# Kernel optimization log

Hardware: AMD Instinct MI355X
Metric: run time of the kernel (lower is better)

The kernel has to match this reference:

```python
import jax, jax.numpy as jnp
import numpy as np

SCALE_POS = 2.0
SCALE_NEG = 40.0
THRESH_POS = 0.5
THRESH_NEG = 0.5
MARGIN = 0.1
EPS = 1e-5


def setup_inputs() -> dict:
    key = jax.random.key(0)
    kf, kl = jax.random.split(key)
    B, D, NUM_CLASSES = 4096, 1024, 64
    feats = jax.random.normal(kf, (B, D), dtype=jnp.float32)
    feats = feats / jnp.linalg.norm(feats, axis=1, keepdims=True)  # L2-normalized embeddings
    labels = jax.random.randint(kl, (B,), 0, NUM_CLASSES, dtype=jnp.int64)
    return {"feats": feats, "labels": labels}


def reference(feats, labels):
    B = feats.shape[0]
    sim = jnp.matmul(feats, feats.T)  # [B, B]
    same = labels[:, None] == labels[None, :]
    pos_mask = same & (sim < 1.0 - EPS)  # drop self / near-duplicate pairs
    neg_mask = ~same

    # hard mining: keep negatives above min positive - margin, positives below max negative + margin
    min_pos = jnp.min(jnp.where(pos_mask, sim, jnp.inf), axis=1)   # [B]
    max_neg = jnp.max(jnp.where(neg_mask, sim, -jnp.inf), axis=1)  # [B]
    neg_sel = neg_mask & (sim + MARGIN > min_pos[:, None])
    pos_sel = pos_mask & (sim - MARGIN < max_neg[:, None])

    pos_sum = jnp.sum(jnp.where(pos_sel, jnp.exp(-SCALE_POS * (sim - THRESH_POS)), 0.0), axis=1)
    neg_sum = jnp.sum(jnp.where(neg_sel, jnp.exp(SCALE_NEG * (sim - THRESH_NEG)), 0.0), axis=1)
    pos_loss = jnp.log1p(pos_sum) / SCALE_POS
    neg_loss = jnp.log1p(neg_sum) / SCALE_NEG

    valid = jnp.any(pos_sel, axis=1) & jnp.any(neg_sel, axis=1)  # rows skipped by original loop
    return jnp.sum(jnp.where(valid, pos_loss + neg_loss, 0.0)) / B
```

## Files before the change

### kernel.cpp

```cpp
#include <hip/hip_runtime.h>

typedef short short8 __attribute__((ext_vector_type(8)));
typedef _Float16 half8 __attribute__((ext_vector_type(8)));
typedef float floatx4 __attribute__((ext_vector_type(4)));
typedef __attribute__((address_space(1))) const void gvoid;
typedef __attribute__((address_space(3))) void svoid;

#define SCALE_POS 2.0f
#define SCALE_NEG 40.0f
#define THRESH 0.5f
#define MARGIN 0.1f
#define EPSV 1e-5f

__device__ __forceinline__ unsigned short f2bf(float f) {
    unsigned u = __float_as_uint(f);
    u += 0x7fffu + ((u >> 16) & 1u);
    return (unsigned short)(u >> 16);
}
__device__ __forceinline__ unsigned f2ord(float f) {
    unsigned u = __float_as_uint(f);
    return (u & 0x80000000u) ? ~u : (u | 0x80000000u);
}
__device__ __forceinline__ float ord2f(unsigned e) {
    unsigned v = (e & 0x80000000u) ? (e & 0x7fffffffu) : ~e;
    return __uint_as_float(v);
}

#define ORD_POS_INF 0xff800000u
#define ORD_NEG_INF 0x007fffffu

__global__ void k_init(const float* __restrict__ feats,
                       unsigned short* __restrict__ fb16,
                       unsigned* __restrict__ minp, unsigned* __restrict__ maxn,
                       float* __restrict__ psum, float* __restrict__ nsum,
                       unsigned* __restrict__ cnts,
                       int total4, int B) {
    int i = blockIdx.x * blockDim.x + threadIdx.x;
    if (i < total4) {
        float4 v = ((const float4*)feats)[i];
        ushort4 o;
        o.x = f2bf(v.x); o.y = f2bf(v.y); o.z = f2bf(v.z); o.w = f2bf(v.w);
        ((ushort4*)fb16)[i] = o;
    }
    if (i < B) {
        minp[i] = ORD_POS_INF;
        maxn[i] = ORD_NEG_INF;
        psum[i] = 0.f;
        nsum[i] = 0.f;
    }
    if (i < 64) cnts[i] = 0;
}

__global__ void __launch_bounds__(128, 2)
k_gemm_h(const unsigned short* __restrict__ fb16,
         const int* __restrict__ labels,
         unsigned* __restrict__ minp_ord,
         unsigned* __restrict__ maxn_ord,
         _Float16* __restrict__ simh,
         int D, int nb) {
    __shared__ __align__(16) unsigned short As[128 * 32];
    __shared__ __align__(16) unsigned short Bs[64 * 32];
    __shared__ int labR[128], labC[64];

    const int bid = blockIdx.x;
    int t = bid >> 1;
    const int h = bid & 1;
    int rb = 0, rem = t;
    while (rem >= nb - rb) { rem -= nb - rb; ++rb; }
    const int cb = rb + rem;
    const int rowBase = rb * 128;
    const int colBase = cb * 128 + h * 64;

    const int tid = threadIdx.x;
    const int lane = tid & 63;
    const int wave = tid >> 6;
    const int q = lane >> 4;
    const int cIn = lane & 15;

    labR[tid] = labels[rowBase + tid];
    if (tid < 64) labC[tid] = labels[colBase + tid];

    const int srow = lane >> 2;
    const int scol = (lane & 3) * 8;
    const unsigned short* gP[6];
    unsigned short* lP[6];
#pragma unroll
    for (int j = 0; j < 6; ++j) {
        const int c = wave * 6 + j;
        const int base = (c < 8) ? (rowBase + c * 16) : (colBase + (c - 8) * 16);
        gP[j] = fb16 + (size_t)(base + srow) * D + scol;
        lP[j] = ((c < 8) ? (As + c * 512) : (Bs + (c - 8) * 512)) + lane * 8;
    }

    int aOff[4], bOff[4];
#pragma unroll
    for (int i = 0; i < 4; ++i) {
        aOff[i] = (wave * 64 + i * 16 + cIn) * 32 + q * 8;
        bOff[i] = (i * 16 + cIn) * 32 + q * 8;
    }

    floatx4 acc[4][4] = {};

    const int KT = D >> 5;
    for (int kt = 0; kt < KT; ++kt) {
        const int kOff = kt * 32;
        __syncthreads();
#pragma unroll
        for (int j = 0; j < 6; ++j)
            __builtin_amdgcn_global_load_lds((gvoid*)(gP[j] + kOff), (svoid*)lP[j], 16, 0, 0);
        __syncthreads();

        short8 a[4], b[4];
#pragma unroll
        for (int i = 0; i < 4; ++i) a[i] = *(const short8*)(As + aOff[i]);
#pragma unroll
        for (int i = 0; i < 4; ++i) b[i] = *(const short8*)(Bs + bOff[i]);
#pragma unroll
        for (int i = 0; i < 4; ++i)
#pragma unroll
            for (int j = 0; j < 4; ++j)
                acc[i][j] = __builtin_amdgcn_mfma_f32_16x16x32_bf16(a[i], b[j], acc[i][j], 0, 0, 0);
    }

    int rLabv[16];
#pragma unroll
    for (int mi = 0; mi < 4; ++mi)
#pragma unroll
        for (int rr = 0; rr < 4; ++rr)
            rLabv[mi * 4 + rr] = labR[wave * 64 + mi * 16 + q * 4 + rr];
    int cLabv[4];
#pragma unroll
    for (int ni = 0; ni < 4; ++ni)
        cLabv[ni] = labC[ni * 16 + cIn];

    {
        half8* dst = (half8*)(simh + (size_t)bid * 8192 + (size_t)tid * 64);
#pragma unroll
        for (int mi = 0; mi < 4; ++mi) {
            half8 h0, h1;
#pragma unroll
            for (int ni = 0; ni < 2; ++ni)
#pragma unroll
                for (int rr = 0; rr < 4; ++rr) {
                    h0[ni * 4 + rr] = (_Float16)acc[mi][ni][rr];
                    h1[ni * 4 + rr] = (_Float16)acc[mi][ni + 2][rr];
                }
            dst[mi * 2] = h0;
            dst[mi * 2 + 1] = h1;
        }
    }

#pragma unroll
    for (int mi = 0; mi < 4; ++mi)
#pragma unroll
        for (int rr = 0; rr < 4; ++rr) {
            const int rLoc = wave * 64 + mi * 16 + q * 4 + rr;
            const int rLab = rLabv[mi * 4 + rr];
            float vmin = 1e30f, vmax = -1e30f;
#pragma unroll
            for (int ni = 0; ni < 4; ++ni) {
                float s = acc[mi][ni][rr];
                if (rLab == cLabv[ni]) {
                    if (s < 1.0f - EPSV) vmin = fminf(vmin, s);
                } else {
                    vmax = fmaxf(vmax, s);
                }
            }
#pragma unroll
            for (int off = 8; off; off >>= 1) {
                vmin = fminf(vmin, __shfl_xor(vmin, off, 16));
                vmax = fmaxf(vmax, __shfl_xor(vmax, off, 16));
            }
            if (cIn == 0) {
                if (vmin < 1e30f) atomicMin(&minp_ord[rowBase + rLoc], f2ord(vmin));
                if (vmax > -1e30f) atomicMax(&maxn_ord[rowBase + rLoc], f2ord(vmax));
            }
        }

    if (rb != cb) {
#pragma unroll
        for (int ni = 0; ni < 4; ++ni) {
            const int cLab = cLabv[ni];
            float vmin = 1e30f, vmax = -1e30f;
#pragma unroll
            for (int mi = 0; mi < 4; ++mi)
#pragma unroll
                for (int rr = 0; rr < 4; ++rr) {
                    float s = acc[mi][ni][rr];
                    if (rLabv[mi * 4 + rr] == cLab) {
                        if (s < 1.0f - EPSV) vmin = fminf(vmin, s);
                    } else {
                        vmax = fmaxf(vmax, s);
                    }
                }
            vmin = fminf(vmin, __shfl_xor(vmin, 16, 64));
            vmin = fminf(vmin, __shfl_xor(vmin, 32, 64));
            vmax = fmaxf(vmax, __shfl_xor(vmax, 16, 64));
            vmax = fmaxf(vmax, __shfl_xor(vmax, 32, 64));
            if (q == 0) {
                const int cLoc = ni * 16 + cIn;
                if (vmin < 1e30f) atomicMin(&minp_ord[colBase + cLoc], f2ord(vmin));
                if (vmax > -1e30f) atomicMax(&maxn_ord[colBase + cLoc], f2ord(vmax));
            }
        }
    }
}

__global__ void __launch_bounds__(256)
k_sum2f(const _Float16* __restrict__ simh,
        const int* __restrict__ labels,
        const unsigned* __restrict__ minp_ord,
        const unsigned* __restrict__ maxn_ord,
        float* __restrict__ psum, float* __restrict__ nsum,
        unsigned* __restrict__ done_cnt,
        float* __restrict__ out,
        int nb, int B) {
    __shared__ int labR[128], labC[128];
    __shared__ float mpR[128], mnR[128], mpC[128], mnC[128];
    __shared__ float red[4];
    __shared__ unsigned lastflag;

    int t = blockIdx.x;
    int rb = 0, rem = t;
    while (rem >= nb - rb) { rem -= nb - rb; ++rb; }
    const int cb = rb + rem;
    const int rowBase = rb * 128;

    const int tid = threadIdx.x;
    const int sub = tid >> 7;
    const int stid = tid & 127;
    const int wave = stid >> 6;
    const int lane = tid & 63;
    const int q = lane >> 4;
    const int cIn = lane & 15;
    const int colBase = cb * 128 + sub * 64;

    if (tid < 128) {
        labR[tid] = labels[rowBase + tid];
        mpR[tid] = ord2f(minp_ord[rowBase + tid]) - MARGIN;
        mnR[tid] = ord2f(maxn_ord[rowBase + tid]) + MARGIN;
    } else {
        const int j = tid - 128;
        labC[j] = labels[cb * 128 + j];
        mpC[j] = ord2f(minp_ord[cb * 128 + j]) - MARGIN;
        mnC[j] = ord2f(maxn_ord[cb * 128 + j]) + MARGIN;
    }
    __syncthreads();

    int cLabv[4];
    float mpCv[4], mnCv[4];
#pragma unroll
    for (int ni = 0; ni < 4; ++ni) {
        const int j = sub * 64 + ni * 16 + cIn;
        cLabv[ni] = labC[j];
        mpCv[ni] = mpC[j];
        mnCv[ni] = mnC[j];
    }

    const half8* src = (const half8*)(simh + (size_t)(2 * t + sub) * 8192 + (size_t)stid * 64);
    half8 hv[8];
#pragma unroll
    for (int v = 0; v < 8; ++v) hv[v] = src[v];

    float cps[4] = {}, cns[4] = {};
    const bool offd = (rb != cb);

#pragma unroll
    for (int mi = 0; mi < 4; ++mi)
#pragma unroll
        for (int rr = 0; rr < 4; ++rr) {
            const int rLoc = wave * 64 + mi * 16 + q * 4 + rr;
            const int rLab = labR[rLoc];
            const float gateN = mpR[rLoc];
            const float gateP = mnR[rLoc];
            float rp = 0.f, rn = 0.f;
#pragma unroll
            for (int ni = 0; ni < 4; ++ni) {
                const int idx = mi * 16 + ni * 4 + rr;
                const float s = (float)hv[idx >> 3][idx & 7];
                if (rLab == cLabv[ni]) {
                    if (s < 1.0f - EPSV) {
                        float ev = __expf(-SCALE_POS * (s - THRESH));
                        if (s < gateP) rp += ev;
                        if (offd && s < mnCv[ni]) cps[ni] += ev;
                    }
                } else {
                    float ev = __expf(SCALE_NEG * (s - THRESH));
                    if (s > gateN) rn += ev;
                    if (offd && s > mpCv[ni]) cns[ni] += ev;
                }
            }
#pragma unroll
            for (int off = 8; off; off >>= 1) {
                rp += __shfl_xor(rp, off, 16);
                rn += __shfl_xor(rn, off, 16);
            }
            if (cIn == 0) {
                if (rp != 0.f) atomicAdd(&psum[rowBase + rLoc], rp);
                if (rn != 0.f) atomicAdd(&nsum[rowBase + rLoc], rn);
            }
        }
    if (offd) {
#pragma unroll
        for (int ni = 0; ni < 4; ++ni) {
            cps[ni] += __shfl_xor(cps[ni], 16, 64);
            cps[ni] += __shfl_xor(cps[ni], 32, 64);
            cns[ni] += __shfl_xor(cns[ni], 16, 64);
            cns[ni] += __shfl_xor(cns[ni], 32, 64);
            if (q == 0) {
                const int cLoc = ni * 16 + cIn;
                if (cps[ni] != 0.f) atomicAdd(&psum[colBase + cLoc], cps[ni]);
                if (cns[ni] != 0.f) atomicAdd(&nsum[colBase + cLoc], cns[ni]);
            }
        }
    }

    __syncthreads();
    if (tid == 0) {
        unsigned prev = __hip_atomic_fetch_add(done_cnt, 1u, __ATOMIC_RELAXED,
                                               __HIP_MEMORY_SCOPE_AGENT);
        lastflag = (prev == (unsigned)(gridDim.x - 1)) ? 1u : 0u;
    }
    __syncthreads();
    if (lastflag) {
        float a = 0.f;
        for (int i = tid; i < B; i += 256) {
            float pv = atomicAdd(&psum[i], 0.0f);
            float nv = atomicAdd(&nsum[i], 0.0f);
            if (pv > 0.f && nv > 0.f)
                a += log1pf(pv) * (1.0f / SCALE_POS) + log1pf(nv) * (1.0f / SCALE_NEG);
        }
#pragma unroll
        for (int off = 32; off; off >>= 1) a += __shfl_down(a, off, 64);
        if ((tid & 63) == 0) red[tid >> 6] = a;
        __syncthreads();
        if (tid == 0) out[0] = (red[0] + red[1] + red[2] + red[3]) / (float)B;
    }
}

extern "C" void kernel_launch(void* const* d_in, const int* in_sizes, int n_in,
                              void* d_out, int out_size, void* d_ws, size_t ws_size,
                              hipStream_t stream) {
    const float* feats = (const float*)d_in[0];
    const int* labels = (const int*)d_in[1];
    const int B = in_sizes[1];
    const int D = in_sizes[0] / B;
    const int nb = B / 128;
    const int NT = nb * (nb + 1) / 2;
    const int NH = NT * 2;
    const int total4 = B * D / 4;

    char* ws = (char*)d_ws;
    unsigned short* fb16 = (unsigned short*)ws;
    size_t off = (size_t)B * D * sizeof(unsigned short);
    unsigned* minp = (unsigned*)(ws + off); off += (size_t)B * 4;
    unsigned* maxn = (unsigned*)(ws + off); off += (size_t)B * 4;
    float* psum = (float*)(ws + off); off += (size_t)B * 4;
    float* nsum = (float*)(ws + off); off += (size_t)B * 4;
    unsigned* cnts = (unsigned*)(ws + off); off += 256;
    _Float16* simh = (_Float16*)(ws + ((off + 255) & ~(size_t)255));
    float* outp = (float*)d_out;

    k_init<<<(total4 + 255) / 256, 256, 0, stream>>>(feats, fb16, minp, maxn,
                                                     psum, nsum, cnts, total4, B);

    k_gemm_h<<<NH, 128, 0, stream>>>(fb16, labels, minp, maxn, simh, D, nb);

    k_sum2f<<<NT, 256, 0, stream>>>(simh, labels, minp, maxn, psum, nsum,
                                    &cnts[1], outp, nb, B);
}
```

Baseline: 146.0 us.

## Fuse GEMM and hard-mining sums into one cooperative kernel with per-block-row barriers

```diff
diff --git a/kernel.cpp b/kernel.cpp
--- a/kernel.cpp
+++ b/kernel.cpp
@@ -28,6 +28,13 @@
 
 #define ORD_POS_INF 0xff800000u
 #define ORD_NEG_INF 0x007fffffu
+
+__device__ __forceinline__ unsigned aload_u32(const unsigned* p) {
+    return __hip_atomic_load(p, __ATOMIC_RELAXED, __HIP_MEMORY_SCOPE_AGENT);
+}
+__device__ __forceinline__ void ainc_u32(unsigned* p) {
+    __hip_atomic_fetch_add(p, 1u, __ATOMIC_RELAXED, __HIP_MEMORY_SCOPE_AGENT);
+}
 
 __global__ void k_init(const float* __restrict__ feats,
                        unsigned short* __restrict__ fb16,
@@ -51,16 +58,21 @@
     if (i < 64) cnts[i] = 0;
 }
 
-__global__ void __launch_bounds__(128, 2)
-k_gemm_h(const unsigned short* __restrict__ fb16,
-         const int* __restrict__ labels,
-         unsigned* __restrict__ minp_ord,
-         unsigned* __restrict__ maxn_ord,
-         _Float16* __restrict__ simh,
-         int D, int nb) {
+__global__ void __launch_bounds__(128)
+k_fused(const unsigned short* __restrict__ fb16,
+        const int* __restrict__ labels,
+        unsigned* __restrict__ minp_ord,
+        unsigned* __restrict__ maxn_ord,
+        float* __restrict__ psum, float* __restrict__ nsum,
+        unsigned* __restrict__ arrive, unsigned* __restrict__ done_cnt,
+        float* __restrict__ out,
+        int D, int nb, int B) {
     __shared__ __align__(16) unsigned short As[128 * 32];
     __shared__ __align__(16) unsigned short Bs[64 * 32];
     __shared__ int labR[128], labC[64];
+    __shared__ float mpR[128], mnR[128], mpC[64], mnC[64];
+    __shared__ float red[2];
+    __shared__ unsigned lastflag;
 
     const int bid = blockIdx.x;
     int t = bid >> 1;
@@ -70,6 +82,7 @@
     const int cb = rb + rem;
     const int rowBase = rb * 128;
     const int colBase = cb * 128 + h * 64;
+    const bool offd = (rb != cb);
 
     const int tid = threadIdx.x;
     const int lane = tid & 63;
@@ -132,23 +145,6 @@
 #pragma unroll
     for (int ni = 0; ni < 4; ++ni)
         cLabv[ni] = labC[ni * 16 + cIn];
-
-    {
-        half8* dst = (half8*)(simh + (size_t)bid * 8192 + (size_t)tid * 64);
-#pragma unroll
-        for (int mi = 0; mi < 4; ++mi) {
-            half8 h0, h1;
-#pragma unroll
-            for (int ni = 0; ni < 2; ++ni)
-#pragma unroll
-                for (int rr = 0; rr < 4; ++rr) {
-                    h0[ni * 4 + rr] = (_Float16)acc[mi][ni][rr];
-                    h1[ni * 4 + rr] = (_Float16)acc[mi][ni + 2][rr];
-                }
-            dst[mi * 2] = h0;
-            dst[mi * 2 + 1] = h1;
-        }
-    }
 
 #pragma unroll
     for (int mi = 0; mi < 4; ++mi)
@@ -177,7 +173,7 @@
             }
         }
 
-    if (rb != cb) {
+    if (offd) {
 #pragma unroll
         for (int ni = 0; ni < 4; ++ni) {
             const int cLab = cLabv[ni];
@@ -204,6 +200,258 @@
             }
         }
     }
+
+    const unsigned target = 2u * (unsigned)nb;
+    __syncthreads();
+    if (tid == 0) {
+        ainc_u32(&arrive[rb]);
+        if (offd) ainc_u32(&arrive[cb]);
+        while (aload_u32(&arrive[rb]) < target) __builtin_amdgcn_s_sleep(2);
+        if (offd)
+            while (aload_u32(&arrive[cb]) < target) __builtin_amdgcn_s_sleep(2);
+    }
+    __syncthreads();
+
+    mpR[tid] = ord2f(aload_u32(&minp_ord[rowBase + tid])) - MARGIN;
+    mnR[tid] = ord2f(aload_u32(&maxn_ord[rowBase + tid])) + MARGIN;
+    if (tid < 64) {
+        mpC[tid] = ord2f(aload_u32(&minp_ord[colBase + tid])) - MARGIN;
+        mnC[tid] = ord2f(aload_u32(&maxn_ord[colBase + tid])) + MARGIN;
+    }
+    __syncthreads();
+
+    float cps[4] = {}, cns[4] = {};
+    float mpCv[4], mnCv[4];
+#pragma unroll
+    for (int ni = 0; ni < 4; ++ni) {
+        mpCv[ni] = mpC[ni * 16 + cIn];
+        mnCv[ni] = mnC[ni * 16 + cIn];
+    }
+#pragma unroll
+    for (int mi = 0; mi < 4; ++mi)
+#pragma unroll
+        for (int rr = 0; rr < 4; ++rr) {
+            const int rLoc = wave * 64 + mi * 16 + q * 4 + rr;
+            const int rLab = rLabv[mi * 4 + rr];
+            const float gateN = mpR[rLoc];
+            const float gateP = mnR[rLoc];
+            float rp = 0.f, rn = 0.f;
+#pragma unroll
+            for (int ni = 0; ni < 4; ++ni) {
+                const float s = acc[mi][ni][rr];
+                if (rLab == cLabv[ni]) {
+                    if (s < 1.0f - EPSV) {
+                        float ev = __expf(-SCALE_POS * (s - THRESH));
+                        if (s < gateP) rp += ev;
+                        if (offd && s < mnCv[ni]) cps[ni] += ev;
+                    }
+                } else {
+                    float ev = __expf(SCALE_NEG * (s - THRESH));
+                    if (s > gateN) rn += ev;
+                    if (offd && s > mpCv[ni]) cns[ni] += ev;
+                }
+            }
+#pragma unroll
+            for (int off = 8; off; off >>= 1) {
+                rp += __shfl_xor(rp, off, 16);
+                rn += __shfl_xor(rn, off, 16);
+            }
+            if (cIn == 0) {
+                if (rp != 0.f) atomicAdd(&psum[rowBase + rLoc], rp);
+                if (rn != 0.f) atomicAdd(&nsum[rowBase + rLoc], rn);
+            }
+        }
+    if (offd) {
+#pragma unroll
+        for (int ni = 0; ni < 4; ++ni) {
+            cps[ni] += __shfl_xor(cps[ni], 16, 64);
+            cps[ni] += __shfl_xor(cps[ni], 32, 64);
+            cns[ni] += __shfl_xor(cns[ni], 16, 64);
+            cns[ni] += __shfl_xor(cns[ni], 32, 64);
+            if (q == 0) {
+                const int cLoc = ni * 16 + cIn;
+                if (cps[ni] != 0.f) atomicAdd(&psum[colBase + cLoc], cps[ni]);
+                if (cns[ni] != 0.f) atomicAdd(&nsum[colBase + cLoc], cns[ni]);
+            }
+        }
+    }
+
+    __syncthreads();
+    if (tid == 0) {
+        unsigned prev = __hip_atomic_fetch_add(done_cnt, 1u, __ATOMIC_RELAXED,
+                                               __HIP_MEMORY_SCOPE_AGENT);
+        lastflag = (prev == gridDim.x - 1) ? 1u : 0u;
+    }
+    __syncthreads();
+    if (lastflag) {
+        float a = 0.f;
+        for (int i = tid; i < B; i += 128) {
+            float pv = atomicAdd(&psum[i], 0.0f);
+            float nv = atomicAdd(&nsum[i], 0.0f);
+            if (pv > 0.f && nv > 0.f)
+                a += log1pf(pv) * (1.0f / SCALE_POS) + log1pf(nv) * (1.0f / SCALE_NEG);
+        }
+#pragma unroll
+        for (int off = 32; off; off >>= 1) a += __shfl_down(a, off, 64);
+        if ((tid & 63) == 0) red[tid >> 6] = a;
+        __syncthreads();
+        if (tid == 0) out[0] = (red[0] + red[1]) / (float)B;
+    }
+}
+
+__global__ void __launch_bounds__(128, 2)
+k_gemm_h(const unsigned short* __restrict__ fb16,
+         const int* __restrict__ labels,
+         unsigned* __restrict__ minp_ord,
+         unsigned* __restrict__ maxn_ord,
+         _Float16* __restrict__ simh,
+         int D, int nb) {
+    __shared__ __align__(16) unsigned short As[128 * 32];
+    __shared__ __align__(16) unsigned short Bs[64 * 32];
+    __shared__ int labR[128], labC[64];
+
+    const int bid = blockIdx.x;
+    int t = bid >> 1;
+    const int h = bid & 1;
+    int rb = 0, rem = t;
+    while (rem >= nb - rb) { rem -= nb - rb; ++rb; }
+    const int cb = rb + rem;
+    const int rowBase = rb * 128;
+    const int colBase = cb * 128 + h * 64;
+
+    const int tid = threadIdx.x;
+    const int lane = tid & 63;
+    const int wave = tid >> 6;
+    const int q = lane >> 4;
+    const int cIn = lane & 15;
+
+    labR[tid] = labels[rowBase + tid];
+    if (tid < 64) labC[tid] = labels[colBase + tid];
+
+    const int srow = lane >> 2;
+    const int scol = (lane & 3) * 8;
+    const unsigned short* gP[6];
+    unsigned short* lP[6];
+#pragma unroll
+    for (int j = 0; j < 6; ++j) {
+        const int c = wave * 6 + j;
+        const int base = (c < 8) ? (rowBase + c * 16) : (colBase + (c - 8) * 16);
+        gP[j] = fb16 + (size_t)(base + srow) * D + scol;
+        lP[j] = ((c < 8) ? (As + c * 512) : (Bs + (c - 8) * 512)) + lane * 8;
+    }
+
+    int aOff[4], bOff[4];
+#pragma unroll
+    for (int i = 0; i < 4; ++i) {
+        aOff[i] = (wave * 64 + i * 16 + cIn) * 32 + q * 8;
+        bOff[i] = (i * 16 + cIn) * 32 + q * 8;
+    }
+
+    floatx4 acc[4][4] = {};
+
+    const int KT = D >> 5;
+    for (int kt = 0; kt < KT; ++kt) {
+        const int kOff = kt * 32;
+        __syncthreads();
+#pragma unroll
+        for (int j = 0; j < 6; ++j)
+            __builtin_amdgcn_global_load_lds((gvoid*)(gP[j] + kOff), (svoid*)lP[j], 16, 0, 0);
+        __syncthreads();
+
+        short8 a[4], b[4];
+#pragma unroll
+        for (int i = 0; i < 4; ++i) a[i] = *(const short8*)(As + aOff[i]);
+#pragma unroll
+        for (int i = 0; i < 4; ++i) b[i] = *(const short8*)(Bs + bOff[i]);
+#pragma unroll
+        for (int i = 0; i < 4; ++i)
+#pragma unroll
+            for (int j = 0; j < 4; ++j)
+                acc[i][j] = __builtin_amdgcn_mfma_f32_16x16x32_bf16(a[i], b[j], acc[i][j], 0, 0, 0);
+    }
+
+    int rLabv[16];
+#pragma unroll
+    for (int mi = 0; mi < 4; ++mi)
+#pragma unroll
+        for (int rr = 0; rr < 4; ++rr)
+            rLabv[mi * 4 + rr] = labR[wave * 64 + mi * 16 + q * 4 + rr];
+    int cLabv[4];
+#pragma unroll
+    for (int ni = 0; ni < 4; ++ni)
+        cLabv[ni] = labC[ni * 16 + cIn];
+
+    {
+        half8* dst = (half8*)(simh + (size_t)bid * 8192 + (size_t)tid * 64);
+#pragma unroll
+        for (int mi = 0; mi < 4; ++mi) {
+            half8 h0, h1;
+#pragma unroll
+            for (int ni = 0; ni < 2; ++ni)
+#pragma unroll
+                for (int rr = 0; rr < 4; ++rr) {
+                    h0[ni * 4 + rr] = (_Float16)acc[mi][ni][rr];
+                    h1[ni * 4 + rr] = (_Float16)acc[mi][ni + 2][rr];
+                }
+            dst[mi * 2] = h0;
+            dst[mi * 2 + 1] = h1;
+        }
+    }
+
+#pragma unroll
+    for (int mi = 0; mi < 4; ++mi)
+#pragma unroll
+        for (int rr = 0; rr < 4; ++rr) {
+            const int rLoc = wave * 64 + mi * 16 + q * 4 + rr;
+            const int rLab = rLabv[mi * 4 + rr];
+            float vmin = 1e30f, vmax = -1e30f;
+#pragma unroll
+            for (int ni = 0; ni < 4; ++ni) {
+                float s = acc[mi][ni][rr];
+                if (rLab == cLabv[ni]) {
+                    if (s < 1.0f - EPSV) vmin = fminf(vmin, s);
+                } else {
+                    vmax = fmaxf(vmax, s);
+                }
+            }
+#pragma unroll
+            for (int off = 8; off; off >>= 1) {
+                vmin = fminf(vmin, __shfl_xor(vmin, off, 16));
+                vmax = fmaxf(vmax, __shfl_xor(vmax, off, 16));
+            }
+            if (cIn == 0) {
+                if (vmin < 1e30f) atomicMin(&minp_ord[rowBase + rLoc], f2ord(vmin));
+                if (vmax > -1e30f) atomicMax(&maxn_ord[rowBase + rLoc], f2ord(vmax));
+            }
+        }
+
+    if (rb != cb) {
+#pragma unroll
+        for (int ni = 0; ni < 4; ++ni) {
+            const int cLab = cLabv[ni];
+            float vmin = 1e30f, vmax = -1e30f;
+#pragma unroll
+            for (int mi = 0; mi < 4; ++mi)
+#pragma unroll
+                for (int rr = 0; rr < 4; ++rr) {
+                    float s = acc[mi][ni][rr];
+                    if (rLabv[mi * 4 + rr] == cLab) {
+                        if (s < 1.0f - EPSV) vmin = fminf(vmin, s);
+                    } else {
+                        vmax = fmaxf(vmax, s);
+                    }
+                }
+            vmin = fminf(vmin, __shfl_xor(vmin, 16, 64));
+            vmin = fminf(vmin, __shfl_xor(vmin, 32, 64));
+            vmax = fmaxf(vmax, __shfl_xor(vmax, 16, 64));
+            vmax = fmaxf(vmax, __shfl_xor(vmax, 32, 64));
+            if (q == 0) {
+                const int cLoc = ni * 16 + cIn;
+                if (vmin < 1e30f) atomicMin(&minp_ord[colBase + cLoc], f2ord(vmin));
+                if (vmax > -1e30f) atomicMax(&maxn_ord[colBase + cLoc], f2ord(vmax));
+            }
+        }
+    }
 }
 
 __global__ void __launch_bounds__(256)
@@ -343,12 +591,12 @@
                               hipStream_t stream) {
     const float* feats = (const float*)d_in[0];
     const int* labels = (const int*)d_in[1];
-    const int B = in_sizes[1];
-    const int D = in_sizes[0] / B;
-    const int nb = B / 128;
+    int B = in_sizes[1];
+    int D = in_sizes[0] / B;
+    int nb = B / 128;
     const int NT = nb * (nb + 1) / 2;
     const int NH = NT * 2;
-    const int total4 = B * D / 4;
+    int total4 = B * D / 4;
 
     char* ws = (char*)d_ws;
     unsigned short* fb16 = (unsigned short*)ws;
@@ -364,8 +612,19 @@
     k_init<<<(total4 + 255) / 256, 256, 0, stream>>>(feats, fb16, minp, maxn,
                                                      psum, nsum, cnts, total4, B);
 
+    unsigned* arrive = cnts;
+    unsigned* done0 = cnts + 32;
+    void* kargs[] = {
+        (void*)&fb16, (void*)&labels, (void*)&minp, (void*)&maxn,
+        (void*)&psum, (void*)&nsum, (void*)&arrive, (void*)&done0,
+        (void*)&outp, (void*)&D, (void*)&nb, (void*)&B
+    };
+    hipError_t err = hipLaunchCooperativeKernel((const void*)(uintptr_t)&k_fused,
+                                                dim3(NH), dim3(128), kargs, 0, stream);
+    if (err == hipSuccess) return;
+    (void)hipGetLastError();
+
     k_gemm_h<<<NH, 128, 0, stream>>>(fb16, labels, minp, maxn, simh, D, nb);
-
     k_sum2f<<<NT, 256, 0, stream>>>(simh, labels, minp, maxn, psum, nsum,
-                                    &cnts[1], outp, nb, B);
-}
+                                    &cnts[33], outp, nb, B);
+}
```

After: 254.1 us. 74.0% more time.
